# Performance work log

Measured on AMD Instinct MI355X. Metric: run time of the kernel, lower is better.

Reference implementation:

```python
import jax, jax.numpy as jnp
import numpy as np

B, S, D = 2, 2048, 512
H, HD = 8, 64
MLP = 2048
WINDOW = 512          # sliding_window_size
N_GLOBAL = 64         # first N_GLOBAL tokens attend/are attended globally
NEG = -1e10


def _xavier(key, shape, fan_in, fan_out):
    lim = np.sqrt(6.0 / (fan_in + fan_out)).astype(np.float32)
    return jax.random.uniform(key, shape, jnp.float32, -lim, lim)


def setup_inputs() -> dict:
    key = jax.random.key(0)
    ks = jax.random.split(key, 8)
    inputs = jax.random.normal(ks[0], (B, S, D), jnp.float32)
    global_mask = jnp.zeros((B, S), jnp.bool_).at[:, :N_GLOBAL].set(True)
    return {
        "inputs": inputs,
        "global_mask": global_mask,
        "ln1_scale": jnp.ones((D,), jnp.float32),
        "ln1_bias": jnp.zeros((D,), jnp.float32),
        "wq": _xavier(ks[1], (D, H, HD), D, H * HD),
        "wk": _xavier(ks[2], (D, H, HD), D, H * HD),
        "wv": _xavier(ks[3], (D, H, HD), D, H * HD),
        "wo": _xavier(ks[4], (H, HD, D), H * HD, D),
        "ln2_scale": jnp.ones((D,), jnp.float32),
        "ln2_bias": jnp.zeros((D,), jnp.float32),
        "w1": _xavier(ks[5], (D, MLP), D, MLP),
        "b1": jnp.zeros((MLP,), jnp.float32),
        "w2": _xavier(ks[6], (MLP, D), MLP, D),
        "b2": jnp.zeros((D,), jnp.float32),
    }


def _layer_norm(x, scale, bias, eps=1e-6):
    m = jnp.mean(x, axis=-1, keepdims=True)
    v = jnp.mean(jnp.square(x - m), axis=-1, keepdims=True)
    return (x - m) * jax.lax.rsqrt(v + eps) * scale + bias


def _longformer_mask(global_mask, seq_len, window):
    # band: |i - j| <= window // 2  (sliding window)
    idx = jnp.arange(seq_len)
    band = jnp.abs(idx[:, None] - idx[None, :]) <= (window // 2)  # [S, S]
    # global rows OR global columns
    glob = global_mask[:, :, None] | global_mask[:, None, :]      # [B, S, S]
    return (band[None, :, :] | glob)[:, None, :, :]               # [B, 1, S, S]


def reference(inputs, global_mask, ln1_scale, ln1_bias, wq, wk, wv, wo,
              ln2_scale, ln2_bias, w1, b1, w2, b2):
    bsz, seq_len, _ = inputs.shape
    head_dim = wq.shape[-1]

    # --- pre-LN + Longformer self-attention ---
    x = _layer_norm(inputs, ln1_scale, ln1_bias)
    q = jnp.einsum('bsd,dhk->bshk', x, wq) / jnp.sqrt(jnp.float32(head_dim))
    k = jnp.einsum('bsd,dhk->bshk', x, wk)
    v = jnp.einsum('bsd,dhk->bshk', x, wv)

    mask = _longformer_mask(global_mask, seq_len, WINDOW)  # [B,1,S,S]
    scores = jnp.einsum('bqhk,bvhk->bhqv', q, k)           # [B,H,S,S]
    scores = jnp.where(mask, scores, NEG)
    attn = jax.nn.softmax(scores, axis=-1)
    ctx = jnp.einsum('bhqv,bvhk->bqhk', attn, v)
    attn_out = jnp.einsum('bqhk,hkd->bqd', ctx, wo)        # output proj, no bias

    x = attn_out + inputs  # residual (dropout deterministic -> identity)

    # --- pre-LN + MLP block ---
    y = _layer_norm(x, ln2_scale, ln2_bias)
    y = jax.nn.gelu(y @ w1 + b1) @ w2 + b2
    return x + y
```

## Files before the change

### kernel.cpp

```cpp
#include <hip/hip_runtime.h>
#include <hip/hip_bf16.h>

typedef __attribute__((ext_vector_type(4))) float f32x4;
typedef __bf16 bf16x8 __attribute__((ext_vector_type(8)));
using bf16 = __hip_bfloat16;

typedef __attribute__((address_space(1))) const void* gptr_t;
typedef __attribute__((address_space(3))) void* lptr_t;
typedef __attribute__((address_space(3))) char* lchar_t;

constexpr int BB = 2, SS = 2048, DDIM = 512, NHEAD = 8, HDIM = 64, MLPD = 2048;
constexpr int NTOK = BB * SS;
constexpr int WHALF = 256;
constexpr int NGLOB = 64;
constexpr float NEGBIG = -1e10f;

constexpr size_t SZ_X1    = (size_t)NTOK * DDIM * 2;
constexpr size_t SZ_WQKVT = (size_t)1536 * DDIM * 2;
constexpr size_t SZ_WOT   = (size_t)DDIM * DDIM * 2;
constexpr size_t SZ_W1T   = (size_t)MLPD * DDIM * 2;
constexpr size_t SZ_W2T   = (size_t)DDIM * MLPD * 2;
constexpr size_t SZ_HEAD  = (size_t)BB * NHEAD * SS * HDIM * 2;
constexpr size_t SZ_QKV   = 3 * SZ_HEAD;
constexpr size_t SZ_CTX   = (size_t)NTOK * DDIM * 2;
constexpr size_t SZ_XRES  = (size_t)NTOK * DDIM * 4;
constexpr size_t SZ_Y1    = (size_t)NTOK * DDIM * 2;
constexpr size_t SZ_H1    = (size_t)NTOK * MLPD * 2;

constexpr size_t OFF_X1    = 0;
constexpr size_t OFF_WQKVT = OFF_X1 + SZ_X1;
constexpr size_t OFF_WOT   = OFF_WQKVT + SZ_WQKVT;
constexpr size_t OFF_W1T   = OFF_WOT + SZ_WOT;
constexpr size_t OFF_W2T   = OFF_W1T + SZ_W1T;
constexpr size_t OFF_QKV   = OFF_W2T + SZ_W2T;
constexpr size_t OFF_CTX   = OFF_QKV + SZ_QKV;
constexpr size_t OFF_XRES  = OFF_CTX + SZ_CTX;
constexpr size_t OFF_Y1    = OFF_XRES + SZ_XRES;
constexpr size_t OFF_H1    = OFF_Y1 + SZ_Y1;
constexpr size_t OFF_GACC  = OFF_H1 + SZ_H1;
constexpr size_t OFF_GL    = OFF_GACC + (size_t)64 * 64 * 64 * 4;

struct TcEnt { const float* src; bf16* dst; int K, N, tiles_x, start; float scale; };
struct PrepArgs {
  TcEnt e[6];
  const float* x; const float* ln_s; const float* ln_b; bf16* ln_out;
};

__global__ void prep_kernel(PrepArgs a) {
  __shared__ __align__(16) bf16 tile[64][65];
  int bid = blockIdx.x;
  int t = threadIdx.x;
  if (bid < 768) {
    int wi = 5;
#pragma unroll
    for (int i = 4; i >= 0; --i)
      if (bid < a.e[i + 1].start) wi = i;
    const TcEnt& E = a.e[wi];
    int local = bid - E.start;
    int bx = local % E.tiles_x, by = local / E.tiles_x;
    int k0 = by * 64, n0 = bx * 64;
    for (int it = 0; it < 8; ++it) {
      int idx = it * 256 + t;
      int r = idx >> 5;
      int c = (idx & 31) * 2;
      float2 v = *(const float2*)&E.src[(size_t)(k0 + r) * E.N + n0 + c];
      tile[c][r] = __float2bfloat16(v.x * E.scale);
      tile[c + 1][r] = __float2bfloat16(v.y * E.scale);
    }
    __syncthreads();
    for (int it = 0; it < 4; ++it) {
      int idx = it * 256 + t;
      int r = idx >> 4;
      int c = (idx & 15) * 4;
      union { ushort u[4]; uint2 v; } pk;
      pk.u[0] = __builtin_bit_cast(ushort, tile[r][c]);
      pk.u[1] = __builtin_bit_cast(ushort, tile[r][c + 1]);
      pk.u[2] = __builtin_bit_cast(ushort, tile[r][c + 2]);
      pk.u[3] = __builtin_bit_cast(ushort, tile[r][c + 3]);
      *(uint2*)&E.dst[(size_t)(n0 + r) * E.K + k0 + c] = pk.v;
    }
  } else {
    int wv = t >> 6;
    int lane = t & 63;
    int row = (bid - 768) * 4 + wv;
    const float* xr = a.x + (size_t)row * DDIM + lane * 8;
    float4 v0 = *(const float4*)(xr);
    float4 v1 = *(const float4*)(xr + 4);
    float vv[8] = {v0.x, v0.y, v0.z, v0.w, v1.x, v1.y, v1.z, v1.w};
    float s = 0.f;
    for (int i = 0; i < 8; ++i) s += vv[i];
    for (int m = 1; m < 64; m <<= 1) s += __shfl_xor(s, m, 64);
    float mean = s * (1.0f / DDIM);
    float vs = 0.f;
    for (int i = 0; i < 8; ++i) { float d = vv[i] - mean; vs += d * d; }
    for (int m = 1; m < 64; m <<= 1) vs += __shfl_xor(vs, m, 64);
    float rstd = rsqrtf(vs * (1.0f / DDIM) + 1e-6f);
    __align__(16) bf16 ov[8];
    int c0 = lane * 8;
    for (int i = 0; i < 8; ++i) {
      float y = (vv[i] - mean) * rstd * a.ln_s[c0 + i] + a.ln_b[c0 + i];
      ov[i] = __float2bfloat16(y);
    }
    *(uint4*)(&a.ln_out[(size_t)row * DDIM + c0]) = *(const uint4*)ov;
  }
}

__global__ void ln_kernel(const float* __restrict__ x, const float* __restrict__ sc,
                          const float* __restrict__ bi, bf16* __restrict__ out) {
  int wv = threadIdx.x >> 6;
  int lane = threadIdx.x & 63;
  int row = blockIdx.x * 4 + wv;
  const float* xr = x + (size_t)row * DDIM + lane * 8;
  float4 v0 = *(const float4*)(xr);
  float4 v1 = *(const float4*)(xr + 4);
  float vv[8] = {v0.x, v0.y, v0.z, v0.w, v1.x, v1.y, v1.z, v1.w};
  float s = 0.f;
  for (int i = 0; i < 8; ++i) s += vv[i];
  for (int m = 1; m < 64; m <<= 1) s += __shfl_xor(s, m, 64);
  float mean = s * (1.0f / DDIM);
  float vs = 0.f;
  for (int i = 0; i < 8; ++i) { float d = vv[i] - mean; vs += d * d; }
  for (int m = 1; m < 64; m <<= 1) vs += __shfl_xor(vs, m, 64);
  float rstd = rsqrtf(vs * (1.0f / DDIM) + 1e-6f);
  __align__(16) bf16 ov[8];
  int c0 = lane * 8;
  for (int i = 0; i < 8; ++i) {
    float y = (vv[i] - mean) * rstd * sc[c0 + i] + bi[c0 + i];
    ov[i] = __float2bfloat16(y);
  }
  *(uint4*)(&out[(size_t)row * DDIM + c0]) = *(const uint4*)ov;
}

template <int BM, int BN, int NP, int EPI>
__global__ __launch_bounds__(256,
    ((2 * NP * (BM + BN) * 128 / 1024) <= 32) ? 4 :
    (((2 * NP * (BM + BN) * 128 / 1024) <= 48) ? 3 : 2))
void gemm_kernel(const bf16* __restrict__ A, const bf16* __restrict__ BT,
                 int M, int N, int K, int gx,
                 const float* __restrict__ ep_add, const float* __restrict__ ep_bias,
                 void* __restrict__ out0) {
  constexpr int AM = BM / 32;
  constexpr int AN = BN / 32;
  constexpr int CA4 = (BM / 8) / 4;
  constexpr int CB4 = (BN / 8) / 4;
  __shared__ __align__(16) bf16 As[2][NP][BM][64];
  __shared__ __align__(16) bf16 Bs[2][NP][BN][64];
  int t = threadIdx.x;
  int wv = t >> 6, lane = t & 63;
  int wr = wv >> 1, wc = wv & 1;
  int g = lane >> 4, lr = lane & 15;
  int sub_r = lane >> 3, sub_s = lane & 7;
  int nwg = gridDim.x;
  int bid = blockIdx.x;
  int swz = (bid & 7) * (nwg >> 3) + (bid >> 3);
  int m0 = (swz / gx) * BM;
  int n0 = (swz % gx) * BN;
  lchar_t asA = (lchar_t)&As[0][0][0][0];
  lchar_t asB = (lchar_t)&Bs[0][0][0][0];

  auto stage = [&](int kt, int bb) {
    int k0 = kt * (64 * NP);
#pragma unroll
    for (int p = 0; p < NP; ++p) {
#pragma unroll
      for (int i = 0; i < CA4; ++i) {
        int c = wv + 4 * i;
        int row = c * 8 + sub_r;
        int cb = sub_s ^ sub_r;
        __builtin_amdgcn_global_load_lds(
            (gptr_t)&A[(size_t)(m0 + row) * K + k0 + p * 64 + cb * 8],
            (lptr_t)(asA + bb * (NP * BM * 128) + p * (BM * 128) + c * 1024), 16, 0, 0);
      }
#pragma unroll
      for (int i = 0; i < CB4; ++i) {
        int c = wv + 4 * i;
        int row = c * 8 + sub_r;
        int cb = sub_s ^ sub_r;
        __builtin_amdgcn_global_load_lds(
            (gptr_t)&BT[(size_t)(n0 + row) * K + k0 + p * 64 + cb * 8],
            (lptr_t)(asB + bb * (NP * BN * 128) + p * (BN * 128) + c * 1024), 16, 0, 0);
      }
    }
  };

  f32x4 acc[AM][AN] = {};
  int NT = K / (64 * NP);
  stage(0, 0);
  asm volatile("s_waitcnt vmcnt(0)" ::: "memory");
  __builtin_amdgcn_s_barrier();
  __builtin_amdgcn_sched_barrier(0);
  for (int kt = 0; kt < NT; ++kt) {
    int bb = kt & 1;
    if (kt + 1 < NT) stage(kt + 1, bb ^ 1);
    const char* Ab = (const char*)&As[0][0][0][0] + bb * (NP * BM * 128);
    const char* Bb = (const char*)&Bs[0][0][0][0] + bb * (NP * BN * 128);
#pragma unroll
    for (int p = 0; p < NP; ++p) {
#pragma unroll
      for (int h = 0; h < 2; ++h) {
        bf16x8 af[AM], bfr[AN];
#pragma unroll
        for (int i = 0; i < AM; ++i) {
          int row = wr * (BM / 2) + i * 16 + lr;
          int sl = (h * 4 + g) ^ (row & 7);
          af[i] = *(const bf16x8*)(Ab + p * (BM * 128) + row * 128 + sl * 16);
        }
#pragma unroll
        for (int j = 0; j < AN; ++j) {
          int row = wc * (BN / 2) + j * 16 + lr;
          int sl = (h * 4 + g) ^ (row & 7);
          bfr[j] = *(const bf16x8*)(Bb + p * (BN * 128) + row * 128 + sl * 16);
        }
#pragma unroll
        for (int i = 0; i < AM; ++i)
#pragma unroll
          for (int j = 0; j < AN; ++j)
            acc[i][j] = __builtin_amdgcn_mfma_f32_16x16x32_bf16(af[i], bfr[j], acc[i][j], 0, 0, 0);
      }
    }
    asm volatile("s_waitcnt vmcnt(0)" ::: "memory");
    __builtin_amdgcn_s_barrier();
    __builtin_amdgcn_sched_barrier(0);
  }
#pragma unroll
  for (int i = 0; i < AM; ++i)
#pragma unroll
    for (int j = 0; j < AN; ++j)
#pragma unroll
      for (int r = 0; r < 4; ++r) {
        int m = m0 + wr * (BM / 2) + i * 16 + g * 4 + r;
        int n = n0 + wc * (BN / 2) + j * 16 + lr;
        float val = acc[i][j][r];
        if constexpr (EPI == 0) {
          bf16* qkv = (bf16*)out0;
          int which = n >> 9;
          int hh = (n >> 6) & 7;
          int hd = n & 63;
          int b = m >> 11, sTok = m & 2047;
          size_t off;
          if (which == 2) {
            off = (size_t)2 * (BB * NHEAD * SS * HDIM) +
                  ((size_t)(b * NHEAD + hh) * HDIM + hd) * SS + sTok;
          } else {
            off = (size_t)which * (BB * NHEAD * SS * HDIM) +
                  ((size_t)(b * NHEAD + hh) * SS + sTok) * HDIM + hd;
          }
          qkv[off] = __float2bfloat16(val);
        } else if constexpr (EPI == 1) {
          ((float*)out0)[(size_t)m * N + n] = val + ep_add[(size_t)m * N + n];
        } else if constexpr (EPI == 2) {
          float xb = val + ep_bias[n];
          float u = 1.5957691216057308f * (xb + 0.044715f * xb * xb * xb);
          float ge = xb / (1.0f + __expf(-u));
          ((bf16*)out0)[(size_t)m * N + n] = __float2bfloat16(ge);
        } else {
          ((float*)out0)[(size_t)m * N + n] = val + ep_bias[n] + ep_add[(size_t)m * N + n];
        }
      }
}

constexpr int NBANDQ = (SS - NGLOB) / 64;
constexpr int NBAND8 = 16 * NBANDQ;
constexpr int NGSPL8 = 16 * 4;
constexpr int NWG8   = NBAND8 + NGSPL8;

__global__ __launch_bounds__(256, 3)
void attn_kernel(const bf16* __restrict__ Qb, const bf16* __restrict__ Kb,
                 const bf16* __restrict__ VTb, bf16* __restrict__ ctx,
                 float* __restrict__ gacc, float* __restrict__ gl) {
  __shared__ __align__(16) bf16 Ks[2][64][64];
  __shared__ __align__(16) bf16 Vs[2][64][64];
  __shared__ __align__(16) bf16 Plds[4][16][72];
  int t = threadIdx.x;
  int w = t >> 6, lane = t & 63;
  int g = lane >> 4, lr = lane & 15;
  int sub_r = lane >> 3, sub_s = lane & 7;
  int bid = blockIdx.x;
  int swz = (bid & 7) * (NWG8 / 8) + (bid >> 3);

  bool isBand = swz < NBAND8;
  int bh, qq0, k0 = 0, sp = 0;
  if (isBand) {
    bh = swz / NBANDQ;
    qq0 = NGLOB + (swz % NBANDQ) * 64;
  } else {
    int gidx = swz - NBAND8;
    bh = gidx >> 2;
    sp = gidx & 3;
    qq0 = 0;
    k0 = sp * (SS / 4);
  }
  int b = bh >> 3, h = bh & 7;
  const bf16* Qh = Qb + (size_t)bh * SS * HDIM;
  const bf16* Kh = Kb + (size_t)bh * SS * HDIM;
  const bf16* VTh = VTb + (size_t)bh * HDIM * SS;
  int qq0w = qq0 + w * 16;

  bf16x8 aq0 = *(const bf16x8*)&Qh[(size_t)(qq0w + lr) * HDIM + g * 8];
  bf16x8 aq1 = *(const bf16x8*)&Qh[(size_t)(qq0w + lr) * HDIM + 32 + g * 8];

  lchar_t ksB = (lchar_t)&Ks[0][0][0];
  lchar_t vsB = (lchar_t)&Vs[0][0][0];
  int cb = sub_s ^ sub_r;

  auto stageKV = [&](int kb, int bb) {
#pragma unroll
    for (int i = 0; i < 2; ++i) {
      int c = w + 4 * i;
      int row = c * 8 + sub_r;
      __builtin_amdgcn_global_load_lds(
          (gptr_t)&Kh[(size_t)(kb + row) * HDIM + cb * 8],
          (lptr_t)(ksB + bb * 8192 + c * 1024), 16, 0, 0);
      __builtin_amdgcn_global_load_lds(
          (gptr_t)&VTh[(size_t)row * SS + kb + cb * 8],
          (lptr_t)(vsB + bb * 8192 + c * 1024), 16, 0, 0);
    }
  };

  float lsum[4] = {0.f, 0.f, 0.f, 0.f};
  f32x4 accO[4] = {};
  const char* ksR = (const char*)&Ks[0][0][0];
  const char* vsR = (const char*)&Vs[0][0][0];

  auto computeT = [&](int kb, int bb, bool domask) {
    const char* Kb_ = ksR + bb * 8192;
    const char* Vb_ = vsR + bb * 8192;
    f32x4 s[4];
#pragma unroll
    for (int sub = 0; sub < 4; ++sub) {
      int row = sub * 16 + lr;
      int sl0 = g ^ (row & 7);
      int sl1 = (4 + g) ^ (row & 7);
      bf16x8 ka = *(const bf16x8*)(Kb_ + row * 128 + sl0 * 16);
      bf16x8 kc = *(const bf16x8*)(Kb_ + row * 128 + sl1 * 16);
      f32x4 z = {};
      z = __builtin_amdgcn_mfma_f32_16x16x32_bf16(aq0, ka, z, 0, 0, 0);
      z = __builtin_amdgcn_mfma_f32_16x16x32_bf16(aq1, kc, z, 0, 0, 0);
      s[sub] = z;
    }
    if (domask) {
#pragma unroll
      for (int sub = 0; sub < 4; ++sub)
#pragma unroll
        for (int r = 0; r < 4; ++r) {
          int i = qq0w + g * 4 + r;
          int d = i - (kb + sub * 16 + lr);
          bool ok = (unsigned)(d + WHALF) <= 2u * WHALF;
          s[sub][r] = ok ? s[sub][r] : NEGBIG;
        }
    }
    float p[4][4];
#pragma unroll
    for (int sub = 0; sub < 4; ++sub)
#pragma unroll
      for (int r = 0; r < 4; ++r) p[sub][r] = __expf(s[sub][r]);
#pragma unroll
    for (int r = 0; r < 4; ++r)
      lsum[r] += (p[0][r] + p[1][r]) + (p[2][r] + p[3][r]);
#pragma unroll
    for (int sub = 0; sub < 4; ++sub)
#pragma unroll
      for (int r = 0; r < 4; ++r)
        Plds[w][g * 4 + r][sub * 16 + lr] = __float2bfloat16(p[sub][r]);
    asm volatile("s_waitcnt lgkmcnt(0)" ::: "memory");
    __builtin_amdgcn_sched_barrier(0);
    bf16x8 paLo = *(const bf16x8*)&Plds[w][lr][g * 8];
    bf16x8 paHi = *(const bf16x8*)&Plds[w][lr][32 + g * 8];
#pragma unroll
    for (int dc = 0; dc < 4; ++dc) {
      int row = dc * 16 + lr;
      int slLo = g ^ (row & 7);
      int slHi = (4 + g) ^ (row & 7);
      bf16x8 vfLo = *(const bf16x8*)(Vb_ + row * 128 + slLo * 16);
      bf16x8 vfHi = *(const bf16x8*)(Vb_ + row * 128 + slHi * 16);
      accO[dc] = __builtin_amdgcn_mfma_f32_16x16x32_bf16(paLo, vfLo, accO[dc], 0, 0, 0);
      accO[dc] = __builtin_amdgcn_mfma_f32_16x16x32_bf16(paHi, vfHi, accO[dc], 0, 0, 0);
    }
  };

  int bs = 0, nt;
  if (isBand) {
    int blo = qq0 - WHALF;
    bs = (blo < NGLOB) ? NGLOB : (blo & ~63);
    int be = qq0 + 64 + WHALF;
    if (be > SS) be = SS;
    nt = 1 + ((be - bs + 63) >> 6);
  } else {
    nt = (SS / 4) / 64;
  }
  auto kb_of = [&](int i) {
    if (isBand) return (i == 0) ? 0 : bs + (i - 1) * 64;
    return k0 + i * 64;
  };

  stageKV(kb_of(0), 0);
  asm volatile("s_waitcnt vmcnt(0)" ::: "memory");
  __builtin_amdgcn_s_barrier();
  __builtin_amdgcn_sched_barrier(0);
  for (int i = 0; i < nt; ++i) {
    int bb = i & 1;
    if (i + 1 < nt) stageKV(kb_of(i + 1), bb ^ 1);
    int kb = kb_of(i);
    bool domask = isBand && (i > 0) &&
                  ((kb < qq0w - 241) || (kb + 63 > qq0w + WHALF));
    computeT(kb, bb, domask);
    asm volatile("s_waitcnt vmcnt(0)" ::: "memory");
    __builtin_amdgcn_s_barrier();
    __builtin_amdgcn_sched_barrier(0);
  }

#pragma unroll
  for (int m = 1; m < 16; m <<= 1)
#pragma unroll
    for (int r = 0; r < 4; ++r) lsum[r] += __shfl_xor(lsum[r], m, 64);

  if (isBand) {
#pragma unroll
    for (int r = 0; r < 4; ++r) {
      float rL = 1.0f / lsum[r];
      int m = b * SS + qq0w + g * 4 + r;
#pragma unroll
      for (int dc = 0; dc < 4; ++dc) {
        int col = h * HDIM + dc * 16 + lr;
        ctx[(size_t)m * DDIM + col] = __float2bfloat16(accO[dc][r] * rL);
      }
    }
  } else {
    int grp = bh * 4 + sp;
#pragma unroll
    for (int r = 0; r < 4; ++r) {
      int rowi = w * 16 + g * 4 + r;
#pragma unroll
      for (int dc = 0; dc < 4; ++dc)
        gacc[((size_t)grp * 64 + rowi) * 64 + dc * 16 + lr] = accO[dc][r];
      if (lr == 0) gl[grp * 64 + rowi] = lsum[r];
    }
  }
}

__global__ __launch_bounds__(64, 4)
void attn_combine_kernel(const float* __restrict__ gacc, const float* __restrict__ gl,
                         bf16* __restrict__ ctx) {
  int bh = blockIdx.x >> 2;
  int rq = blockIdx.x & 3;
  int b = bh >> 3, h = bh & 7;
  int c = threadIdx.x;
  for (int rr = 0; rr < 16; ++rr) {
    int r = rq * 16 + rr;
    float L = 0.f, val = 0.f;
    for (int s2 = 0; s2 < 4; ++s2) {
      L += gl[(bh * 4 + s2) * 64 + r];
      val += gacc[((size_t)(bh * 4 + s2) * 64 + r) * 64 + c];
    }
    ctx[(size_t)(b * SS + r) * DDIM + h * HDIM + c] = __float2bfloat16(val / L);
  }
}

extern "C" void kernel_launch(void* const* d_in, const int* in_sizes, int n_in,
                              void* d_out, int out_size, void* d_ws, size_t ws_size,
                              hipStream_t stream) {
  const float* inputs = (const float*)d_in[0];
  const float* ln1_s = (const float*)d_in[2];
  const float* ln1_b = (const float*)d_in[3];
  const float* wq = (const float*)d_in[4];
  const float* wk = (const float*)d_in[5];
  const float* wv = (const float*)d_in[6];
  const float* wo = (const float*)d_in[7];
  const float* ln2_s = (const float*)d_in[8];
  const float* ln2_b = (const float*)d_in[9];
  const float* w1 = (const float*)d_in[10];
  const float* b1 = (const float*)d_in[11];
  const float* w2 = (const float*)d_in[12];
  const float* b2 = (const float*)d_in[13];

  char* ws = (char*)d_ws;
  bf16* x1    = (bf16*)(ws + OFF_X1);
  bf16* wqkvT = (bf16*)(ws + OFF_WQKVT);
  bf16* woT   = (bf16*)(ws + OFF_WOT);
  bf16* w1T   = (bf16*)(ws + OFF_W1T);
  bf16* w2T   = (bf16*)(ws + OFF_W2T);
  bf16* qkv   = (bf16*)(ws + OFF_QKV);
  bf16* ctx   = (bf16*)(ws + OFF_CTX);
  float* xres = (float*)(ws + OFF_XRES);
  bf16* y1    = (bf16*)(ws + OFF_Y1);
  bf16* h1    = (bf16*)(ws + OFF_H1);
  float* gacc = (float*)(ws + OFF_GACC);
  float* gl   = (float*)(ws + OFF_GL);
  size_t headsz = (size_t)BB * NHEAD * SS * HDIM;

  PrepArgs pa;
  pa.e[0] = {wq, wqkvT,                       512, 512,  8,   0, 0.125f};
  pa.e[1] = {wk, wqkvT + (size_t)512 * 512,   512, 512,  8,  64, 1.f};
  pa.e[2] = {wv, wqkvT + (size_t)1024 * 512,  512, 512,  8, 128, 1.f};
  pa.e[3] = {wo, woT,                         512, 512,  8, 192, 1.f};
  pa.e[4] = {w1, w1T,                         512, 2048, 32, 256, 1.f};
  pa.e[5] = {w2, w2T,                         2048, 512, 8, 512, 1.f};
  pa.x = inputs; pa.ln_s = ln1_s; pa.ln_b = ln1_b; pa.ln_out = x1;
  prep_kernel<<<768 + NTOK / 4, 256, 0, stream>>>(pa);

  gemm_kernel<64, 128, 1, 0><<<12 * 64, 256, 0, stream>>>(x1, wqkvT, NTOK, 1536, 512, 12, nullptr, nullptr, qkv);
  attn_kernel<<<NWG8, 256, 0, stream>>>(qkv, qkv + headsz, qkv + 2 * headsz, ctx, gacc, gl);
  attn_combine_kernel<<<64, 64, 0, stream>>>(gacc, gl, ctx);
  gemm_kernel<64, 64, 2, 1><<<8 * 64, 256, 0, stream>>>(ctx, woT, NTOK, 512, 512, 8, inputs, nullptr, xres);
  ln_kernel<<<NTOK / 4, 256, 0, stream>>>(xres, ln2_s, ln2_b, y1);
  gemm_kernel<128, 128, 1, 2><<<16 * 32, 256, 0, stream>>>(y1, w1T, NTOK, 2048, 512, 16, nullptr, b1, h1);
  gemm_kernel<64, 64, 2, 3><<<8 * 64, 256, 0, stream>>>(h1, w2T, NTOK, 512, 2048, 8, xres, b2, (float*)d_out);
}
```

Before: 95.53 us.

## Widen attention KV tiles from 64 to 128 keys per iteration

Each attention loop iteration now stages and processes 128 keys instead of 64, which doubles the K/V shared-memory buffers and changes the swizzle layout for V to 16 slots. This halves the number of barrier/wait iterations per workgroup. The band start is realigned to 128, so the first tile (keys 0-127) now needs a mask mode that keeps the global columns plus band entries. The cost is more LDS, which lowers launch bounds occupancy from 3 to 2, plus extra masked work at the band edges.

```diff
diff --git a/kernel.cpp b/kernel.cpp
--- a/kernel.cpp
+++ b/kernel.cpp
@@ -264,17 +264,16 @@
 constexpr int NGSPL8 = 16 * 4;
 constexpr int NWG8   = NBAND8 + NGSPL8;
 
-__global__ __launch_bounds__(256, 3)
+__global__ __launch_bounds__(256, 2)
 void attn_kernel(const bf16* __restrict__ Qb, const bf16* __restrict__ Kb,
                  const bf16* __restrict__ VTb, bf16* __restrict__ ctx,
                  float* __restrict__ gacc, float* __restrict__ gl) {
-  __shared__ __align__(16) bf16 Ks[2][64][64];
-  __shared__ __align__(16) bf16 Vs[2][64][64];
+  __shared__ __align__(16) bf16 Ks[2][128][64];
+  __shared__ __align__(16) bf16 Vs[2][64][128];
   __shared__ __align__(16) bf16 Plds[4][16][72];
   int t = threadIdx.x;
   int w = t >> 6, lane = t & 63;
   int g = lane >> 4, lr = lane & 15;
-  int sub_r = lane >> 3, sub_s = lane & 7;
   int bid = blockIdx.x;
   int swz = (bid & 7) * (NWG8 / 8) + (bid >> 3);
 
@@ -301,19 +300,24 @@
 
   lchar_t ksB = (lchar_t)&Ks[0][0][0];
   lchar_t vsB = (lchar_t)&Vs[0][0][0];
-  int cb = sub_s ^ sub_r;
+
+  int kst_sub = lane >> 3, kst_slot = lane & 7;
+  int vst_sub = lane >> 4, vst_slot = lane & 15;
 
   auto stageKV = [&](int kb, int bb) {
 #pragma unroll
-    for (int i = 0; i < 2; ++i) {
-      int c = w + 4 * i;
-      int row = c * 8 + sub_r;
+    for (int i = 0; i < 4; ++i) {
+      int c = w * 4 + i;
+      int krow = c * 8 + kst_sub;
+      int kcb = kst_slot ^ (krow & 7);
       __builtin_amdgcn_global_load_lds(
-          (gptr_t)&Kh[(size_t)(kb + row) * HDIM + cb * 8],
-          (lptr_t)(ksB + bb * 8192 + c * 1024), 16, 0, 0);
+          (gptr_t)&Kh[(size_t)(kb + krow) * HDIM + kcb * 8],
+          (lptr_t)(ksB + bb * 16384 + c * 1024), 16, 0, 0);
+      int vrow = c * 4 + vst_sub;
+      int vcb = vst_slot ^ (vrow & 15);
       __builtin_amdgcn_global_load_lds(
-          (gptr_t)&VTh[(size_t)row * SS + kb + cb * 8],
-          (lptr_t)(vsB + bb * 8192 + c * 1024), 16, 0, 0);
+          (gptr_t)&VTh[(size_t)vrow * SS + kb + vcb * 8],
+          (lptr_t)(vsB + bb * 16384 + c * 1024), 16, 0, 0);
     }
   };
 
@@ -322,12 +326,12 @@
   const char* ksR = (const char*)&Ks[0][0][0];
   const char* vsR = (const char*)&Vs[0][0][0];
 
-  auto computeT = [&](int kb, int bb, bool domask) {
-    const char* Kb_ = ksR + bb * 8192;
-    const char* Vb_ = vsR + bb * 8192;
-    f32x4 s[4];
-#pragma unroll
-    for (int sub = 0; sub < 4; ++sub) {
+  auto computeT = [&](int kb, int bb, int mode) {
+    const char* Kb_ = ksR + bb * 16384;
+    const char* Vb_ = vsR + bb * 16384;
+    f32x4 s[8];
+#pragma unroll
+    for (int sub = 0; sub < 8; ++sub) {
       int row = sub * 16 + lr;
       int sl0 = g ^ (row & 7);
       int sl1 = (4 + g) ^ (row & 7);
@@ -338,59 +342,69 @@
       z = __builtin_amdgcn_mfma_f32_16x16x32_bf16(aq1, kc, z, 0, 0, 0);
       s[sub] = z;
     }
-    if (domask) {
-#pragma unroll
-      for (int sub = 0; sub < 4; ++sub)
+    if (mode != 0) {
+#pragma unroll
+      for (int sub = 0; sub < 8; ++sub)
 #pragma unroll
         for (int r = 0; r < 4; ++r) {
           int i = qq0w + g * 4 + r;
-          int d = i - (kb + sub * 16 + lr);
+          int j = kb + sub * 16 + lr;
+          int d = i - j;
           bool ok = (unsigned)(d + WHALF) <= 2u * WHALF;
+          if (mode == 2) ok = ok || (j < NGLOB);
           s[sub][r] = ok ? s[sub][r] : NEGBIG;
         }
     }
-    float p[4][4];
-#pragma unroll
-    for (int sub = 0; sub < 4; ++sub)
+    float p[8][4];
+#pragma unroll
+    for (int sub = 0; sub < 8; ++sub)
 #pragma unroll
       for (int r = 0; r < 4; ++r) p[sub][r] = __expf(s[sub][r]);
 #pragma unroll
     for (int r = 0; r < 4; ++r)
-      lsum[r] += (p[0][r] + p[1][r]) + (p[2][r] + p[3][r]);
-#pragma unroll
-    for (int sub = 0; sub < 4; ++sub)
-#pragma unroll
-      for (int r = 0; r < 4; ++r)
-        Plds[w][g * 4 + r][sub * 16 + lr] = __float2bfloat16(p[sub][r]);
-    asm volatile("s_waitcnt lgkmcnt(0)" ::: "memory");
-    __builtin_amdgcn_sched_barrier(0);
-    bf16x8 paLo = *(const bf16x8*)&Plds[w][lr][g * 8];
-    bf16x8 paHi = *(const bf16x8*)&Plds[w][lr][32 + g * 8];
-#pragma unroll
-    for (int dc = 0; dc < 4; ++dc) {
-      int row = dc * 16 + lr;
-      int slLo = g ^ (row & 7);
-      int slHi = (4 + g) ^ (row & 7);
-      bf16x8 vfLo = *(const bf16x8*)(Vb_ + row * 128 + slLo * 16);
-      bf16x8 vfHi = *(const bf16x8*)(Vb_ + row * 128 + slHi * 16);
-      accO[dc] = __builtin_amdgcn_mfma_f32_16x16x32_bf16(paLo, vfLo, accO[dc], 0, 0, 0);
-      accO[dc] = __builtin_amdgcn_mfma_f32_16x16x32_bf16(paHi, vfHi, accO[dc], 0, 0, 0);
+      lsum[r] += ((p[0][r] + p[1][r]) + (p[2][r] + p[3][r])) +
+                 ((p[4][r] + p[5][r]) + (p[6][r] + p[7][r]));
+#pragma unroll
+    for (int pp = 0; pp < 2; ++pp) {
+#pragma unroll
+      for (int sub = 0; sub < 4; ++sub)
+#pragma unroll
+        for (int r = 0; r < 4; ++r)
+          Plds[w][g * 4 + r][sub * 16 + lr] = __float2bfloat16(p[pp * 4 + sub][r]);
+      asm volatile("s_waitcnt lgkmcnt(0)" ::: "memory");
+      __builtin_amdgcn_sched_barrier(0);
+      bf16x8 paLo = *(const bf16x8*)&Plds[w][lr][g * 8];
+      bf16x8 paHi = *(const bf16x8*)&Plds[w][lr][32 + g * 8];
+#pragma unroll
+      for (int dc = 0; dc < 4; ++dc) {
+        int vrow = dc * 16 + lr;
+        int slLo = (pp * 8 + g) ^ (vrow & 15);
+        int slHi = (pp * 8 + 4 + g) ^ (vrow & 15);
+        bf16x8 vfLo = *(const bf16x8*)(Vb_ + vrow * 256 + slLo * 16);
+        bf16x8 vfHi = *(const bf16x8*)(Vb_ + vrow * 256 + slHi * 16);
+        accO[dc] = __builtin_amdgcn_mfma_f32_16x16x32_bf16(paLo, vfLo, accO[dc], 0, 0, 0);
+        accO[dc] = __builtin_amdgcn_mfma_f32_16x16x32_bf16(paHi, vfHi, accO[dc], 0, 0, 0);
+      }
+      if (pp == 0) {
+        asm volatile("s_waitcnt lgkmcnt(0)" ::: "memory");
+        __builtin_amdgcn_sched_barrier(0);
+      }
     }
   };
 
   int bs = 0, nt;
   if (isBand) {
     int blo = qq0 - WHALF;
-    bs = (blo < NGLOB) ? NGLOB : (blo & ~63);
+    bs = (blo < 128) ? 128 : (blo & ~127);
     int be = qq0 + 64 + WHALF;
     if (be > SS) be = SS;
-    nt = 1 + ((be - bs + 63) >> 6);
+    nt = 1 + ((be - bs + 127) >> 7);
   } else {
-    nt = (SS / 4) / 64;
+    nt = (SS / 4) / 128;
   }
   auto kb_of = [&](int i) {
-    if (isBand) return (i == 0) ? 0 : bs + (i - 1) * 64;
-    return k0 + i * 64;
+    if (isBand) return (i == 0) ? 0 : bs + (i - 1) * 128;
+    return k0 + i * 128;
   };
 
   stageKV(kb_of(0), 0);
@@ -401,9 +415,16 @@
     int bb = i & 1;
     if (i + 1 < nt) stageKV(kb_of(i + 1), bb ^ 1);
     int kb = kb_of(i);
-    bool domask = isBand && (i > 0) &&
-                  ((kb < qq0w - 241) || (kb + 63 > qq0w + WHALF));
-    computeT(kb, bb, domask);
+    int mode;
+    if (!isBand) {
+      mode = 0;
+    } else if (i == 0) {
+      mode = 2;
+    } else {
+      bool edge = (kb < qq0w - WHALF) || (kb + 127 > qq0w + 15 + WHALF);
+      mode = edge ? 1 : 0;
+    }
+    computeT(kb, bb, mode);
     asm volatile("s_waitcnt vmcnt(0)" ::: "memory");
     __builtin_amdgcn_s_barrier();
     __builtin_amdgcn_sched_barrier(0);
```

Measured after the change: 101.6 us. 6.4% more time.
